# Kernel optimization log

Measured on AMD Instinct MI355X. Metric: run time of the kernel, lower is better.

The kernel has to match this reference:

```python
import jax, jax.numpy as jnp
import numpy as np

DEV_VDW, VDW_N, MAXV, MINV, DM_MIN = 0.2, 6.0, 0.0356, 0.0178, 0.5


def setup_inputs() -> dict:
    key = jax.random.key(0)
    ks = iter(jax.random.split(key, 64))
    B, N1, N2, D, L = 8, 128, 256, 128, 3
    f = jnp.float32
    nrm = lambda shape, s=0.05: jax.random.normal(next(ks), shape, f) * s
    ligand_h = jax.random.normal(next(ks), (B, N1, 54), f)
    target_h = jax.random.normal(next(ks), (B, N2, 54), f)
    def adj(n):
        a = (jax.random.uniform(next(ks), (B, n, n)) < 0.08).astype(f)
        a = jnp.maximum(a, jnp.swapaxes(a, 1, 2))
        return jnp.maximum(a, jnp.eye(n, dtype=f))
    ligand_adj = adj(N1)
    target_adj = adj(N2)
    interaction_indice = jax.random.uniform(next(ks), (B, 3, N1, N2), f)
    ligand_pos = jax.random.normal(next(ks), (B, N1, 3), f) * 2.0
    target_pos = jax.random.normal(next(ks), (B, N2, 3), f) * 4.0
    rotor = jax.random.uniform(next(ks), (B,), f) * 10.0
    ligand_vdw_radii = 1.2 + 0.8 * jax.random.uniform(next(ks), (B, N1), f)
    target_vdw_radii = 1.2 + 0.8 * jax.random.uniform(next(ks), (B, N2), f)
    return dict(
        ligand_h=ligand_h, ligand_adj=ligand_adj, target_h=target_h, target_adj=target_adj,
        interaction_indice=interaction_indice, ligand_pos=ligand_pos, target_pos=target_pos,
        rotor=rotor, ligand_vdw_radii=ligand_vdw_radii, target_vdw_radii=target_vdw_radii,
        ligand_valid=jnp.ones((B, N1), f), target_valid=jnp.ones((B, N2), f),
        ligand_non_metal=jnp.ones((B, N1), f), target_non_metal=jnp.ones((B, N2), f),
        emb_w=nrm((54, D)),
        gat_w=nrm((L, D, D)), gat_b=jnp.zeros((L, D), f), gat_att=nrm((L, D, D)),
        gat_gate_w=nrm((L, 2 * D, 1)), gat_gate_b=jnp.zeros((L, 1), f),
        int_wt_w=nrm((L, D, D)), int_wt_b=jnp.zeros((L, D), f),
        int_mt_w=nrm((L, D, D)), int_mt_b=jnp.zeros((L, D), f),
        gru_w_ih=nrm((L, 3 * D, D)), gru_w_hh=nrm((L, 3 * D, D)),
        gru_b_ih=jnp.zeros((L, 3 * D), f), gru_b_hh=jnp.zeros((L, 3 * D), f),
        A_w1=nrm((2 * D, D)), A_b1=jnp.zeros((D,), f), A_w2=nrm((D, 1)), A_b2=jnp.zeros((1,), f),
        B_w1=nrm((2 * D, D)), B_b1=jnp.zeros((D,), f), B_w2=nrm((D, 1)), B_b2=jnp.zeros((1,), f),
        hbond_coeff=jnp.array([1.0], f), hydrophobic_coeff=jnp.array([0.5], f),
        rotor_coeff=jnp.array([0.5], f),
    )


def reference(ligand_h, ligand_adj, target_h, target_adj, interaction_indice, ligand_pos,
              target_pos, rotor, ligand_vdw_radii, target_vdw_radii, ligand_valid,
              target_valid, ligand_non_metal, target_non_metal, emb_w, gat_w, gat_b,
              gat_att, gat_gate_w, gat_gate_b, int_wt_w, int_wt_b, int_mt_w, int_mt_b,
              gru_w_ih, gru_w_hh, gru_b_ih, gru_b_hh, A_w1, A_b1, A_w2, A_b2, B_w1, B_b1,
              B_w2, B_b2, hbond_coeff, hydrophobic_coeff, rotor_coeff):
    B, D, L = ligand_h.shape[0], emb_w.shape[1], gat_w.shape[0]

    def dist(lpos):
        diff = lpos[:, :, None, :] - target_pos[:, None, :, :]
        dm = jnp.sqrt((diff * diff).sum(-1) + 1e-10)
        return jnp.where(dm < DM_MIN, 1e10, dm)

    dm = dist(ligand_pos)

    def gat(x, adj, i):
        nt = x @ gat_w[i] + gat_b[i]                                   # [B,N,D]
        ea = jnp.einsum('bjl,bkl->bjk', nt @ gat_att[i], nt)
        ea = ea + jnp.swapaxes(ea, 1, 2)
        aw = jax.nn.softmax(jnp.where(adj > 1e-6, ea, -9e15), axis=-1) * adj
        out = jax.nn.relu(jnp.einsum('bij,bjd->bid', aw, nt))
        gate = jax.nn.sigmoid(jnp.concatenate([x, out], -1) @ gat_gate_w[i] + gat_gate_b[i])
        return gate * x + (1.0 - gate) * out

    lh = ligand_h @ emb_w
    th = target_h @ emb_w
    for i in range(L):
        lh = gat(lh, ligand_adj, i)
        th = gat(th, target_adj, i)

    adj12 = jax.lax.stop_gradient(dm)
    adj12 = jnp.where(adj12 > 5.0, 0.0, adj12)
    adj12 = jnp.where(adj12 > 1e-3, 1.0, 0.0)
    adj21 = jnp.swapaxes(adj12, 1, 2)

    def inter(a1, a2, ev, i):
        t1 = a1 @ int_wt_w[i] + int_wt_b[i]
        m2 = a2 @ int_mt_w[i] + int_mt_b[i]                            # [B,N2,D]
        t2 = (m2[:, None, :, :] * ev[..., None]).max(axis=2)           # [B,N1,D]
        msg = jax.nn.relu(t1 + t2)
        gi = msg @ gru_w_ih[i].T + gru_b_ih[i]
        gh = a1 @ gru_w_hh[i].T + gru_b_hh[i]
        i_r, i_z, i_n = jnp.split(gi, 3, -1)
        h_r, h_z, h_n = jnp.split(gh, 3, -1)
        r = jax.nn.sigmoid(i_r + h_r)
        z = jax.nn.sigmoid(i_z + h_z)
        n = jnp.tanh(i_n + r * h_n)
        return (1.0 - z) * n + z * a1

    for i in range(L):
        lh, th = inter(lh, th, adj12, i), inter(th, lh, adj21, i)

    N1, N2 = lh.shape[1], th.shape[1]
    h_cat = jnp.concatenate([
        jnp.broadcast_to(lh[:, :, None, :], (B, N1, N2, D)),
        jnp.broadcast_to(th[:, None, :, :], (B, N1, N2, D))], -1)      # [B,N1,N2,2D]

    A_raw = jax.nn.sigmoid(jax.nn.relu(h_cat @ A_w1 + A_b1) @ A_w2 + A_b2)[..., 0]
    B_raw = jnp.tanh(jax.nn.relu(h_cat @ B_w1 + B_b1) @ B_w2 + B_b2)[..., 0] * DEV_VDW
    dm0 = ligand_vdw_radii[:, :, None] + target_vdw_radii[:, None, :] + B_raw
    valid_pair = ligand_non_metal[:, :, None] * target_non_metal[:, None, :]
    A_vdw = A_raw * (MAXV - MINV) + MINV

    def energies_of(dm):
        dm0c = jnp.where(dm0 < 1e-4, 1.0, dm0)
        r6 = (dm0c / dm) ** VDW_N
        evdw = A_vdw * (jnp.minimum(r6 * r6 - 2.0 * r6, 100.0) * valid_pair)
        vdw_val = evdw.sum((1, 2))[:, None]
        dmd = dm - dm0
        def hb(Aind):
            r = jnp.clip(dmd * Aind / -0.7, 0.0, 1.0) * -(hbond_coeff[0] * hbond_coeff[0])
            return r.sum((1, 2))[:, None]
        hbond = hb(interaction_indice[:, 0])
        metal = hb(interaction_indice[:, 1])
        hp = jnp.clip((-dmd + 1.5) * interaction_indice[:, 2], 0.0, 1.0)
        hp = hp * -(hydrophobic_coeff[0] * hydrophobic_coeff[0])
        e = jnp.concatenate([vdw_val, hbond, metal, hp.sum((1, 2))[:, None]], -1)
        return e / (1.0 + rotor_coeff[0] * rotor_coeff[0] * rotor[:, None])

    energies = energies_of(dm)
    esum = lambda p: energies_of(dist(p)).sum()
    g = jax.grad(esum)(ligand_pos)
    der1 = (g.sum(1) ** 2).mean()
    der2 = -jax.grad(lambda p: jax.grad(esum)(p).sum())(ligand_pos).sum((1, 2)).mean()
    return energies, der1, der2
```

## Files before the change

kernel.cpp:

```cpp
#include <hip/hip_runtime.h>
#include <math.h>

#define BB 8
#define N1C 128
#define N2C 256
#define DC 128
#define NHC 54
#define ROWS_L 1024
#define ROWS_T 2048
#define ROWS_ALL 3072

__device__ __forceinline__ float wredSum(float v) {
#pragma unroll
  for (int o = 32; o > 0; o >>= 1) v += __shfl_down(v, o);
  return v;
}
__device__ float blockSum(float v) {
  __shared__ float red[9];
  v = wredSum(v);
  int lane = threadIdx.x & 63, wid = threadIdx.x >> 6;
  __syncthreads();
  if (lane == 0) red[wid] = v;
  __syncthreads();
  if (threadIdx.x == 0) {
    float s = 0.f;
    int nw = (blockDim.x + 63) >> 6;
    for (int i = 0; i < nw; ++i) s += red[i];
    red[8] = s;
  }
  __syncthreads();
  return red[8];
}

__global__ __launch_bounds__(128) void k_emb(const float* __restrict__ LH,
                                             const float* __restrict__ TH,
                                             const float* __restrict__ W,
                                             float* __restrict__ H0) {
  int r0 = blockIdx.x * 4;
  __shared__ float xs[4][NHC];
  for (int t = threadIdx.x; t < 4 * NHC; t += 128) {
    int rr = r0 + t / NHC, c = t % NHC;
    xs[t / NHC][c] = (rr < ROWS_L) ? LH[(long)rr * NHC + c]
                                   : TH[(long)(rr - ROWS_L) * NHC + c];
  }
  __syncthreads();
  int d = threadIdx.x;
  float a0 = 0.f, a1 = 0.f, a2 = 0.f, a3 = 0.f;
#pragma unroll 6
  for (int k = 0; k < NHC; ++k) {
    float wv = W[(long)k * DC + d];
    a0 += xs[0][k] * wv;
    a1 += xs[1][k] * wv;
    a2 += xs[2][k] * wv;
    a3 += xs[3][k] * wv;
  }
  H0[(long)(r0 + 0) * DC + d] = a0;
  H0[(long)(r0 + 1) * DC + d] = a1;
  H0[(long)(r0 + 2) * DC + d] = a2;
  H0[(long)(r0 + 3) * DC + d] = a3;
}

__global__ __launch_bounds__(128) void k_wfuse(const float* __restrict__ GWp,
                                               const float* __restrict__ GBp,
                                               const float* __restrict__ ATT,
                                               float* __restrict__ WA,
                                               float* __restrict__ bA) {
  int l = blockIdx.y;
  const float* Wl = GWp + (long)l * DC * DC;
  const float* Al = ATT + (long)l * DC * DC;
  int d = threadIdx.x;
  if (blockIdx.x == 32) {
    float acc = 0.f;
#pragma unroll 8
    for (int m = 0; m < DC; ++m) acc += GBp[l * DC + m] * Al[(long)m * DC + d];
    bA[l * DC + d] = acc;
    return;
  }
  int r0 = blockIdx.x * 4;
  __shared__ float xs[4][DC];
  for (int t = threadIdx.x; t < 4 * DC; t += 128)
    xs[t >> 7][t & 127] = Wl[(long)r0 * DC + t];
  __syncthreads();
  float a0 = 0.f, a1 = 0.f, a2 = 0.f, a3 = 0.f;
#pragma unroll 8
  for (int m = 0; m < DC; ++m) {
    float av = Al[(long)m * DC + d];
    a0 += xs[0][m] * av;
    a1 += xs[1][m] * av;
    a2 += xs[2][m] * av;
    a3 += xs[3][m] * av;
  }
  float* out = WA + (long)l * DC * DC + (long)r0 * DC + d;
  out[0] = a0;
  out[DC] = a1;
  out[2 * DC] = a2;
  out[3 * DC] = a3;
}

__global__ __launch_bounds__(256) void k_lin2h(
    const float* __restrict__ X, const float* __restrict__ W1,
    const float* __restrict__ b1, const float* __restrict__ W2,
    const float* __restrict__ b2, float* __restrict__ Y1, float* __restrict__ Y2,
    int rpb, int trans) {
  int r0 = blockIdx.x * 4;
  __shared__ float xs[4][DC];
  int tid = threadIdx.x;
  for (int t = tid; t < 4 * DC; t += 256)
    xs[t >> 7][t & 127] = X[(long)r0 * DC + t];
  __syncthreads();
  int h = tid >> 7, d = tid & 127;
  const float* W = h ? W2 : W1;
  const float* bp = h ? b2 : b1;
  float* Y = h ? Y2 : Y1;
  float a0 = 0.f, a1 = 0.f, a2 = 0.f, a3 = 0.f;
#pragma unroll 16
  for (int k = 0; k < DC; ++k) {
    float wv = W[(long)k * DC + d];
    a0 += xs[0][k] * wv;
    a1 += xs[1][k] * wv;
    a2 += xs[2][k] * wv;
    a3 += xs[3][k] * wv;
  }
  float bv = bp ? bp[d] : 0.f;
  float v[4] = {a0 + bv, a1 + bv, a2 + bv, a3 + bv};
  if (!trans) {
#pragma unroll
    for (int r = 0; r < 4; ++r) Y[(long)(r0 + r) * DC + d] = v[r];
  } else {
    int b = r0 / rpb, rin = r0 - b * rpb;
#pragma unroll
    for (int r = 0; r < 4; ++r)
      Y[((long)b * DC + d) * rpb + rin + r] = v[r];
  }
}

template <int N>
__global__ __launch_bounds__(256) void k_ea(const float* __restrict__ NTp,
                                            const float* __restrict__ E1p,
                                            const float* __restrict__ ADJ,
                                            float* __restrict__ EAp,
                                            int baseRow) {
  const int D = DC;
  int b = blockIdx.z;
  int j0 = blockIdx.y * 16, k0 = blockIdx.x * 16;
  int tj = threadIdx.y, tk = threadIdx.x;
  __shared__ float e1j[16][17], ntj[16][17], e1k[16][17], ntk[16][17];
  const float* E1b = E1p + (long)(baseRow + b * N) * D;
  const float* NTb = NTp + (long)(baseRow + b * N) * D;
  float acc = 0.f;
  for (int kk = 0; kk < D; kk += 16) {
    e1j[tj][tk] = E1b[(long)(j0 + tj) * D + kk + tk];
    ntj[tj][tk] = NTb[(long)(j0 + tj) * D + kk + tk];
    e1k[tj][tk] = E1b[(long)(k0 + tj) * D + kk + tk];
    ntk[tj][tk] = NTb[(long)(k0 + tj) * D + kk + tk];
    __syncthreads();
#pragma unroll
    for (int t = 0; t < 16; ++t)
      acc += e1j[tj][t] * ntk[tk][t] + ntj[tj][t] * e1k[tk][t];
    __syncthreads();
  }
  long idx = (long)b * N * N + (long)(j0 + tj) * N + k0 + tk;
  float ad = ADJ[idx];
  EAp[idx] = (ad > 1e-6f) ? acc : -9e15f;
}

__global__ __launch_bounds__(512) void k_smagg(
    const float* __restrict__ EAL, const float* __restrict__ EAT,
    const float* __restrict__ NTp, const float* __restrict__ Xp,
    const float* __restrict__ GW, const float* __restrict__ GB,
    float* __restrict__ Y) {
  int z = blockIdx.z;
  int N = z ? N2C : N1C;
  if (blockIdx.x * 8 >= N) return;
  int ls = z ? 8 : 7;
  int baseRow = z ? ROWS_L : 0;
  const float* EA = z ? EAT : EAL;
  int b = blockIdx.y, i0 = blockIdx.x * 8;
  __shared__ float ps[8][N2C + 4];
  __shared__ float col[32][DC + 4];
  __shared__ float red[8][2];
  int tid = threadIdx.x;
  const float* EAb = EA + (long)b * N * N + (long)i0 * N;
  for (int t = tid; t < 8 * N; t += 512)
    ps[t >> ls][t & (N - 1)] = EAb[t];
  __syncthreads();
  {
    int r = tid >> 6, l = tid & 63;
    float m = -INFINITY;
    for (int k = l; k < N; k += 64) m = fmaxf(m, ps[r][k]);
#pragma unroll
    for (int o = 32; o > 0; o >>= 1) m = fmaxf(m, __shfl_xor(m, o));
    float s = 0.f;
    for (int k = l; k < N; k += 64) {
      float p = expf(ps[r][k] - m);
      ps[r][k] = p;
      s += p;
    }
#pragma unroll
    for (int o = 32; o > 0; o >>= 1) s += __shfl_xor(s, o);
    float inv = 1.f / s;
    for (int k = l; k < N; k += 64) ps[r][k] *= inv;
  }
  int d = tid & 127, ro = tid >> 7;
  float acc[2] = {0.f, 0.f};
  const float* NTb = NTp + (long)(baseRow + b * N) * DC;
  for (int k0 = 0; k0 < N; k0 += 32) {
    __syncthreads();
    for (int t = tid; t < 32 * DC; t += 512)
      col[t >> 7][t & 127] = NTb[(long)(k0 + (t >> 7)) * DC + (t & 127)];
    __syncthreads();
#pragma unroll 8
    for (int kk = 0; kk < 32; ++kk) {
      float cv = col[kk][d];
      acc[0] = fmaf(ps[ro][k0 + kk], cv, acc[0]);
      acc[1] = fmaf(ps[ro + 4][k0 + kk], cv, acc[1]);
    }
  }
  float gwd = GW[d], gwo = GW[DC + d];
  float xv[2], ov[2], part[2];
#pragma unroll
  for (int q = 0; q < 2; ++q) {
    int r = ro + 4 * q;
    float o = fmaxf(acc[q], 0.f);
    ov[q] = o;
    float x = Xp[(long)(baseRow + b * N + i0 + r) * DC + d];
    xv[q] = x;
    part[q] = x * gwd + o * gwo;
  }
  int wid = tid >> 6;
#pragma unroll
  for (int q = 0; q < 2; ++q) {
    float v = wredSum(part[q]);
    if ((tid & 63) == 0) red[wid][q] = v;
  }
  __syncthreads();
  float gb = GB[0];
#pragma unroll
  for (int q = 0; q < 2; ++q) {
    int r = ro + 4 * q;
    float s = red[2 * ro][q] + red[2 * ro + 1][q];
    float g = 1.f / (1.f + expf(-(s + gb)));
    Y[(long)(baseRow + b * N + i0 + r) * DC + d] = g * xv[q] + (1.f - g) * ov[q];
  }
}

__global__ void k_adj12(const float* __restrict__ LP, const float* __restrict__ TP,
                        float* __restrict__ AD) {
  long idx = (long)blockIdx.x * blockDim.x + threadIdx.x;
  if (idx >= (long)BB * N1C * N2C) return;
  int j = idx & (N2C - 1);
  long t = idx >> 8;
  int i = (int)(t & (N1C - 1));
  int b = (int)(t >> 7);
  float dx = LP[((long)b * N1C + i) * 3 + 0] - TP[((long)b * N2C + j) * 3 + 0];
  float dy = LP[((long)b * N1C + i) * 3 + 1] - TP[((long)b * N2C + j) * 3 + 1];
  float dz = LP[((long)b * N1C + i) * 3 + 2] - TP[((long)b * N2C + j) * 3 + 2];
  float d = sqrtf(dx * dx + dy * dy + dz * dz + 1e-10f);
  if (d < 0.5f) d = 1e10f;
  AD[idx] = (d <= 5.0f && d > 1e-3f) ? 1.f : 0.f;
}

__global__ __launch_bounds__(256) void k_msg2z(const float* __restrict__ T1,
                                               const float* __restrict__ M2,
                                               const float* __restrict__ EV,
                                               float* __restrict__ MSG) {
  int z = blockIdx.z, b = blockIdx.y;
  int Ni = z ? N2C : N1C, Nj = z ? N1C : N2C;
  int t1off = z ? ROWS_L : 0, m2off = z ? 0 : ROWS_L;
  long ev_is = z ? 1L : (long)N2C, ev_js = z ? (long)N2C : 1L;
  int i0 = blockIdx.x * 8;
  if (i0 >= Ni) return;
  __shared__ float m2s[32][DC];
  __shared__ float evs[8][32];
  int d = threadIdx.x & 127, io = threadIdx.x >> 7;
  float acc[4];
#pragma unroll
  for (int q = 0; q < 4; ++q) acc[q] = -INFINITY;
  const float* M2b = M2 + (long)(m2off + b * Nj) * DC;
  const float* EVb = EV + (long)b * (N1C * N2C);
  for (int j0 = 0; j0 < Nj; j0 += 32) {
    __syncthreads();
    for (int t = threadIdx.x; t < 32 * DC; t += 256)
      m2s[t >> 7][t & 127] = M2b[(long)(j0 + (t >> 7)) * DC + (t & 127)];
    for (int t = threadIdx.x; t < 8 * 32; t += 256)
      evs[t >> 5][t & 31] =
          EVb[(long)(i0 + (t >> 5)) * ev_is + (long)(j0 + (t & 31)) * ev_js];
    __syncthreads();
#pragma unroll 8
    for (int jj = 0; jj < 32; ++jj) {
      float m2v = m2s[jj][d];
#pragma unroll
      for (int q = 0; q < 4; ++q)
        acc[q] = fmaxf(acc[q], m2v * evs[io + 2 * q][jj]);
    }
  }
#pragma unroll
  for (int q = 0; q < 4; ++q) {
    int i = i0 + io + 2 * q;
    long row = t1off + (long)b * Ni + i;
    MSG[row * DC + d] = fmaxf(T1[row * DC + d] + acc[q], 0.f);
  }
}

__global__ __launch_bounds__(384) void k_gruf(
    const float* __restrict__ MSGp, const float* __restrict__ Hp,
    const float* __restrict__ WihT, const float* __restrict__ WhhT,
    const float* __restrict__ bih, const float* __restrict__ bhh,
    float* __restrict__ Y) {
  const int D = DC;
  int r0 = blockIdx.x * 4;
  __shared__ float xs_t[DC][4], hs_t[DC][4];
  __shared__ float gis[4][384], ghs[4][384];
  int tid = threadIdx.x;
  for (int t = tid; t < 4 * DC; t += 384) {
    int r = t >> 7, c = t & 127;
    xs_t[c][r] = MSGp[(long)(r0 + r) * D + c];
    hs_t[c][r] = Hp[(long)(r0 + r) * D + c];
  }
  __syncthreads();
  int dd = tid;
  float ai[4] = {0.f, 0.f, 0.f, 0.f}, ah[4] = {0.f, 0.f, 0.f, 0.f};
#pragma unroll 8
  for (int k = 0; k < DC; ++k) {
    float4 xv = *reinterpret_cast<const float4*>(&xs_t[k][0]);
    float4 hv = *reinterpret_cast<const float4*>(&hs_t[k][0]);
    float wi = WihT[(long)k * 384 + dd];
    float wh = WhhT[(long)k * 384 + dd];
    ai[0] = fmaf(xv.x, wi, ai[0]);
    ai[1] = fmaf(xv.y, wi, ai[1]);
    ai[2] = fmaf(xv.z, wi, ai[2]);
    ai[3] = fmaf(xv.w, wi, ai[3]);
    ah[0] = fmaf(hv.x, wh, ah[0]);
    ah[1] = fmaf(hv.y, wh, ah[1]);
    ah[2] = fmaf(hv.z, wh, ah[2]);
    ah[3] = fmaf(hv.w, wh, ah[3]);
  }
  float bi = bih[dd], bh = bhh[dd];
#pragma unroll
  for (int r = 0; r < 4; ++r) {
    gis[r][dd] = ai[r] + bi;
    ghs[r][dd] = ah[r] + bh;
  }
  __syncthreads();
  for (int t = tid; t < 4 * DC; t += 384) {
    int r = t >> 7, d = t & 127;
    float ir = gis[r][d], iz = gis[r][d + 128], inn = gis[r][d + 256];
    float hr = ghs[r][d], hz = ghs[r][d + 128], hn = ghs[r][d + 256];
    float rg = 1.f / (1.f + expf(-(ir + hr)));
    float zg = 1.f / (1.f + expf(-(iz + hz)));
    float ng = tanhf(inn + rg * hn);
    Y[(long)(r0 + r) * D + d] = (1.f - zg) * ng + zg * hs_t[d][r];
  }
}

__global__ void k_tall(const float* __restrict__ IH, const float* __restrict__ HH,
                       float* __restrict__ GIHT, float* __restrict__ GHHT) {
  long idx = (long)blockIdx.x * 256 + threadIdx.x;
  if (idx >= 6L * 49152) return;
  int a = (int)(idx / 49152);
  int rem = (int)(idx % 49152);
  int l = a >> 1, whh = a & 1;
  int c = rem / 384, rr = rem % 384;
  const float* src = (whh ? HH : IH) + (long)l * 49152;
  float* dst = (whh ? GHHT : GIHT) + (long)l * 49152;
  dst[(long)c * 384 + rr] = src[(long)rr * 128 + c];
}

__global__ __launch_bounds__(256) void k_pair(
    const float* __restrict__ UA, const float* __restrict__ VAT,
    const float* __restrict__ UB, const float* __restrict__ VBT,
    const float* __restrict__ AW2, const float* __restrict__ AB2,
    const float* __restrict__ BW2, const float* __restrict__ BB2,
    const float* __restrict__ LP, const float* __restrict__ TP,
    const float* __restrict__ LVDW, const float* __restrict__ TVDW,
    const float* __restrict__ LNM, const float* __restrict__ TNM,
    const float* __restrict__ II, const float* __restrict__ HBC,
    const float* __restrict__ HPC, float* __restrict__ PART) {
  const int D = DC, N1 = N1C, N2 = N2C;
  int i = blockIdx.x, b = blockIdx.y, j = threadIdx.x;
  __shared__ float ua[128], ub[128], wa2[128], wb2[128];
  if (j < 128) {
    long rb = ((long)b * N1 + i) * D + j;
    ua[j] = UA[rb];
    ub[j] = UB[rb];
    wa2[j] = AW2[j];
    wb2[j] = BW2[j];
  }
  __syncthreads();
  const float* vat = VAT + (long)b * D * N2;
  const float* vbt = VBT + (long)b * D * N2;
  float dotA = 0.f, dotB = 0.f;
#pragma unroll 8
  for (int d = 0; d < D; ++d) {
    dotA += fmaxf(ua[d] + vat[(long)d * N2 + j], 0.f) * wa2[d];
    dotB += fmaxf(ub[d] + vbt[(long)d * N2 + j], 0.f) * wb2[d];
  }
  float A_raw = 1.f / (1.f + expf(-(dotA + AB2[0])));
  float A_vdw = A_raw * (0.0356f - 0.0178f) + 0.0178f;
  float B_raw = tanhf(dotB + BB2[0]) * 0.2f;

  float lx = LP[((long)b * N1 + i) * 3 + 0];
  float ly = LP[((long)b * N1 + i) * 3 + 1];
  float lz = LP[((long)b * N1 + i) * 3 + 2];
  float tx = TP[((long)b * N2 + j) * 3 + 0];
  float ty = TP[((long)b * N2 + j) * 3 + 1];
  float tz = TP[((long)b * N2 + j) * 3 + 2];
  float dx = lx - tx, dy = ly - ty, dz = lz - tz;
  float s2 = dx * dx + dy * dy + dz * dz + 1e-10f;
  float draw = sqrtf(s2);
  bool clamped = draw < 0.5f;
  float dmv = clamped ? 1e10f : draw;

  float dm0 = LVDW[b * N1 + i] + TVDW[b * N2 + j] + B_raw;
  float dm0c = (dm0 < 1e-4f) ? 1.f : dm0;
  float valid = LNM[b * N1 + i] * TNM[b * N2 + j];

  float rr = dm0c / dmv;
  float r2 = rr * rr, r6 = r2 * r2 * r2;
  float fv = r6 * r6 - 2.f * r6;
  float evdw = A_vdw * (fminf(fv, 100.f) * valid);

  float dmd = dmv - dm0;
  long ii0 = ((long)b * 3) * N1 * N2 + (long)i * N2 + j;
  float I0 = II[ii0];
  float I1 = II[ii0 + (long)N1 * N2];
  float I2 = II[ii0 + 2L * N1 * N2];
  float hb2 = HBC[0] * HBC[0], hp2 = HPC[0] * HPC[0];
  float u0 = dmd * I0 / (-0.7f);
  float u1 = dmd * I1 / (-0.7f);
  float vv = (1.5f - dmd) * I2;
  float ehb = fminf(fmaxf(u0, 0.f), 1.f) * (-hb2);
  float emt = fminf(fmaxf(u1, 0.f), 1.f) * (-hb2);
  float ehp = fminf(fmaxf(vv, 0.f), 1.f) * (-hp2);

  float gx = 0.f, gy = 0.f, gz = 0.f, d2t = 0.f;
  if (!clamped) {
    float Ep = 0.f, Epp = 0.f;
    if (fv < 100.f) {
      float c = A_vdw * valid;
      Ep += c * (-12.f) * r6 * (r6 - 1.f) / draw;
      Epp += c * r6 * (156.f * r6 - 84.f) / s2;
    }
    if (u0 > 0.f && u0 < 1.f) Ep += hb2 * I0 * (1.f / 0.7f);
    if (u1 > 0.f && u1 < 1.f) Ep += hb2 * I1 * (1.f / 0.7f);
    if (vv > 0.f && vv < 1.f) Ep += hp2 * I2;
    float invd = 1.f / draw;
    gx = Ep * dx * invd;
    gy = Ep * dy * invd;
    gz = Ep * dz * invd;
    float T = dx + dy + dz;
    float tt = T * T / s2;
    d2t = Epp * tt + Ep * (3.f - tt) * invd;
  }

  float o0 = blockSum(evdw);
  float o1 = blockSum(ehb);
  float o2 = blockSum(emt);
  float o3 = blockSum(ehp);
  float o4 = blockSum(gx);
  float o5 = blockSum(gy);
  float o6 = blockSum(gz);
  float o7 = blockSum(d2t);
  if (j == 0) {
    float* p = PART + ((long)b * N1 + i) * 8;
    p[0] = o0; p[1] = o1; p[2] = o2; p[3] = o3;
    p[4] = o4; p[5] = o5; p[6] = o6; p[7] = o7;
  }
}

__global__ void k_final(const float* __restrict__ PART, const float* __restrict__ ROT,
                        const float* __restrict__ RC, float* __restrict__ OUT) {
  const int N1 = N1C;
  __shared__ float s[8][8];
  int t = threadIdx.x;
  if (t < 64) {
    int b = t >> 3, k1 = t & 7;
    float acc = 0.f;
    for (int i = 0; i < N1; ++i) acc += PART[((long)b * N1 + i) * 8 + k1];
    s[b][k1] = acc;
  }
  __syncthreads();
  if (t == 0) {
    float rcc = RC[0] * RC[0];
    float der1 = 0.f, der2 = 0.f;
    for (int b = 0; b < 8; ++b) {
      float w = 1.f / (1.f + rcc * ROT[b]);
      OUT[b * 4 + 0] = s[b][0] * w;
      OUT[b * 4 + 1] = s[b][1] * w;
      OUT[b * 4 + 2] = s[b][2] * w;
      OUT[b * 4 + 3] = s[b][3] * w;
      for (int c = 0; c < 3; ++c) {
        float S = s[b][4 + c] * w;
        der1 += S * S;
      }
      der2 += s[b][7] * w;
    }
    OUT[32] = der1 / 24.f;
    OUT[33] = -der2 / 8.f;
  }
}

extern "C" void kernel_launch(void* const* d_in, const int* in_sizes, int n_in,
                              void* d_out, int out_size, void* d_ws, size_t ws_size,
                              hipStream_t stream) {
  (void)in_sizes; (void)n_in; (void)out_size; (void)ws_size;
  const int D = DC;

  const float* ligand_h   = (const float*)d_in[0];
  const float* ligand_adj = (const float*)d_in[1];
  const float* target_h   = (const float*)d_in[2];
  const float* target_adj = (const float*)d_in[3];
  const float* inter_ind  = (const float*)d_in[4];
  const float* ligand_pos = (const float*)d_in[5];
  const float* target_pos = (const float*)d_in[6];
  const float* rotor      = (const float*)d_in[7];
  const float* lvdw       = (const float*)d_in[8];
  const float* tvdw       = (const float*)d_in[9];
  const float* lnm        = (const float*)d_in[12];
  const float* tnm        = (const float*)d_in[13];
  const float* emb_w      = (const float*)d_in[14];
  const float* gat_w      = (const float*)d_in[15];
  const float* gat_b      = (const float*)d_in[16];
  const float* gat_att    = (const float*)d_in[17];
  const float* gat_gate_w = (const float*)d_in[18];
  const float* gat_gate_b = (const float*)d_in[19];
  const float* int_wt_w   = (const float*)d_in[20];
  const float* int_wt_b   = (const float*)d_in[21];
  const float* int_mt_w   = (const float*)d_in[22];
  const float* int_mt_b   = (const float*)d_in[23];
  const float* gru_w_ih   = (const float*)d_in[24];
  const float* gru_w_hh   = (const float*)d_in[25];
  const float* gru_b_ih   = (const float*)d_in[26];
  const float* gru_b_hh   = (const float*)d_in[27];
  const float* A_w1       = (const float*)d_in[28];
  const float* A_b1       = (const float*)d_in[29];
  const float* A_w2       = (const float*)d_in[30];
  const float* A_b2       = (const float*)d_in[31];
  const float* B_w1       = (const float*)d_in[32];
  const float* B_b1       = (const float*)d_in[33];
  const float* B_w2       = (const float*)d_in[34];
  const float* B_b2       = (const float*)d_in[35];
  const float* hb_c       = (const float*)d_in[36];
  const float* hp_c       = (const float*)d_in[37];
  const float* rc_c       = (const float*)d_in[38];

  float* w = (float*)d_ws;
  auto take = [&](size_t n) { float* p = w; w += n; return p; };
  float* H0    = take((size_t)ROWS_ALL * DC);
  float* H1    = take((size_t)ROWS_ALL * DC);
  float* NT    = take((size_t)ROWS_ALL * DC);
  float* E1    = take((size_t)ROWS_ALL * DC);
  float* EAL   = take((size_t)BB * N1C * N1C);
  float* EAT   = take((size_t)BB * N2C * N2C);
  float* ADJ12 = take((size_t)BB * N1C * N2C);
  float* WA    = take((size_t)3 * DC * DC);
  float* bA    = take((size_t)3 * DC);
  float* GIHT  = take((size_t)3 * DC * 384);
  float* GHHT  = take((size_t)3 * DC * 384);
  float* PART  = take((size_t)BB * N1C * 8);
  float* T1  = NT;
  float* M2  = E1;
  float* MSG = EAT;
  float* UA  = EAL;
  float* UB  = EAT;
  float* VAT = NT;
  float* VBT = E1;

  k_adj12<<<(BB * N1C * N2C + 255) / 256, 256, 0, stream>>>(ligand_pos,
                                                            target_pos, ADJ12);
  k_emb<<<ROWS_ALL / 4, 128, 0, stream>>>(ligand_h, target_h, emb_w, H0);
  k_wfuse<<<dim3(33, 3), 128, 0, stream>>>(gat_w, gat_b, gat_att, WA, bA);

  float *cur = H0, *alt = H1;

  for (int l = 0; l < 3; ++l) {
    k_lin2h<<<ROWS_ALL / 4, 256, 0, stream>>>(
        cur, gat_w + (size_t)l * D * D, gat_b + l * D, WA + (size_t)l * D * D,
        bA + l * D, NT, E1, 1, 0);
    k_ea<N1C><<<dim3(N1C / 16, N1C / 16, BB), dim3(16, 16), 0, stream>>>(
        NT, E1, ligand_adj, EAL, 0);
    k_ea<N2C><<<dim3(N2C / 16, N2C / 16, BB), dim3(16, 16), 0, stream>>>(
        NT, E1, target_adj, EAT, ROWS_L);
    k_smagg<<<dim3(N2C / 8, BB, 2), 512, 0, stream>>>(
        EAL, EAT, NT, cur, gat_gate_w + l * 2 * D, gat_gate_b + l, alt);
    float* t = cur; cur = alt; alt = t;
  }

  k_tall<<<(6 * 49152 + 255) / 256, 256, 0, stream>>>(gru_w_ih, gru_w_hh, GIHT,
                                                      GHHT);

  for (int l = 0; l < 3; ++l) {
    k_lin2h<<<ROWS_ALL / 4, 256, 0, stream>>>(
        cur, int_wt_w + (size_t)l * D * D, int_wt_b + l * D,
        int_mt_w + (size_t)l * D * D, int_mt_b + l * D, T1, M2, 1, 0);
    k_msg2z<<<dim3(N2C / 8, BB, 2), 256, 0, stream>>>(T1, M2, ADJ12, MSG);
    k_gruf<<<ROWS_ALL / 4, 384, 0, stream>>>(MSG, cur, GIHT + (size_t)l * D * 384,
                                             GHHT + (size_t)l * D * 384,
                                             gru_b_ih + l * 384,
                                             gru_b_hh + l * 384, alt);
    float* t = cur; cur = alt; alt = t;
  }

  k_lin2h<<<ROWS_L / 4, 256, 0, stream>>>(cur, A_w1, A_b1, B_w1, B_b1, UA, UB,
                                          1, 0);
  k_lin2h<<<ROWS_T / 4, 256, 0, stream>>>(cur + (size_t)ROWS_L * DC,
                                          A_w1 + D * D, nullptr, B_w1 + D * D,
                                          nullptr, VAT, VBT, N2C, 1);

  k_pair<<<dim3(N1C, BB), 256, 0, stream>>>(UA, VAT, UB, VBT, A_w2, A_b2, B_w2,
                                            B_b2, ligand_pos, target_pos, lvdw,
                                            tvdw, lnm, tnm, inter_ind, hb_c,
                                            hp_c, PART);

  k_final<<<1, 256, 0, stream>>>(PART, rotor, rc_c, (float*)d_out);
}
```

Before: 374.0 us.

## Merge prep kernels, register-tile attention GEMM, vectorize msg and lin2h inner loops

```diff
diff --git a/kernel.cpp b/kernel.cpp
--- a/kernel.cpp
+++ b/kernel.cpp
@@ -32,69 +32,96 @@
   return red[8];
 }
 
-__global__ __launch_bounds__(128) void k_emb(const float* __restrict__ LH,
-                                             const float* __restrict__ TH,
-                                             const float* __restrict__ W,
-                                             float* __restrict__ H0) {
-  int r0 = blockIdx.x * 4;
-  __shared__ float xs[4][NHC];
-  for (int t = threadIdx.x; t < 4 * NHC; t += 128) {
-    int rr = r0 + t / NHC, c = t % NHC;
-    xs[t / NHC][c] = (rr < ROWS_L) ? LH[(long)rr * NHC + c]
-                                   : TH[(long)(rr - ROWS_L) * NHC + c];
-  }
-  __syncthreads();
-  int d = threadIdx.x;
-  float a0 = 0.f, a1 = 0.f, a2 = 0.f, a3 = 0.f;
+__global__ __launch_bounds__(256) void k_prep(
+    const float* __restrict__ LP, const float* __restrict__ TP,
+    float* __restrict__ AD, const float* __restrict__ LH,
+    const float* __restrict__ TH, const float* __restrict__ EW,
+    float* __restrict__ H0, const float* __restrict__ GWp,
+    const float* __restrict__ GBp, const float* __restrict__ ATT,
+    float* __restrict__ WA, float* __restrict__ bA,
+    const float* __restrict__ IH, const float* __restrict__ HH,
+    float* __restrict__ GIHT, float* __restrict__ GHHT) {
+  int bid = blockIdx.x, tid = threadIdx.x;
+  if (bid < 1024) {
+    long idx = (long)bid * 256 + tid;
+    int j = idx & (N2C - 1);
+    long t = idx >> 8;
+    int i = (int)(t & (N1C - 1));
+    int b = (int)(t >> 7);
+    float dx = LP[((long)b * N1C + i) * 3 + 0] - TP[((long)b * N2C + j) * 3 + 0];
+    float dy = LP[((long)b * N1C + i) * 3 + 1] - TP[((long)b * N2C + j) * 3 + 1];
+    float dz = LP[((long)b * N1C + i) * 3 + 2] - TP[((long)b * N2C + j) * 3 + 2];
+    float d = sqrtf(dx * dx + dy * dy + dz * dz + 1e-10f);
+    if (d < 0.5f) d = 1e10f;
+    AD[idx] = (d <= 5.0f && d > 1e-3f) ? 1.f : 0.f;
+  } else if (bid < 1024 + 384) {
+    int r0 = (bid - 1024) * 8;
+    __shared__ float xs[8][NHC];
+    for (int t = tid; t < 8 * NHC; t += 256) {
+      int rr = r0 + t / NHC, c = t % NHC;
+      xs[t / NHC][c] = (rr < ROWS_L) ? LH[(long)rr * NHC + c]
+                                     : TH[(long)(rr - ROWS_L) * NHC + c];
+    }
+    __syncthreads();
+    int d = tid & 127, rb = (tid >> 7) * 4;
+    float a[4] = {0.f, 0.f, 0.f, 0.f};
 #pragma unroll 6
-  for (int k = 0; k < NHC; ++k) {
-    float wv = W[(long)k * DC + d];
-    a0 += xs[0][k] * wv;
-    a1 += xs[1][k] * wv;
-    a2 += xs[2][k] * wv;
-    a3 += xs[3][k] * wv;
-  }
-  H0[(long)(r0 + 0) * DC + d] = a0;
-  H0[(long)(r0 + 1) * DC + d] = a1;
-  H0[(long)(r0 + 2) * DC + d] = a2;
-  H0[(long)(r0 + 3) * DC + d] = a3;
-}
-
-__global__ __launch_bounds__(128) void k_wfuse(const float* __restrict__ GWp,
-                                               const float* __restrict__ GBp,
-                                               const float* __restrict__ ATT,
-                                               float* __restrict__ WA,
-                                               float* __restrict__ bA) {
-  int l = blockIdx.y;
-  const float* Wl = GWp + (long)l * DC * DC;
-  const float* Al = ATT + (long)l * DC * DC;
-  int d = threadIdx.x;
-  if (blockIdx.x == 32) {
-    float acc = 0.f;
+    for (int k = 0; k < NHC; ++k) {
+      float wv = EW[(long)k * DC + d];
+#pragma unroll
+      for (int r = 0; r < 4; ++r) a[r] += xs[rb + r][k] * wv;
+    }
+#pragma unroll
+    for (int r = 0; r < 4; ++r) H0[(long)(r0 + rb + r) * DC + d] = a[r];
+  } else if (bid < 1024 + 384 + 99) {
+    int q = bid - 1408;
+    int l = q / 33, bx = q % 33;
+    const float* Wl = GWp + (long)l * DC * DC;
+    const float* Al = ATT + (long)l * DC * DC;
+    if (bx == 32) {
+      if (tid < 128) {
+        float acc = 0.f;
 #pragma unroll 8
-    for (int m = 0; m < DC; ++m) acc += GBp[l * DC + m] * Al[(long)m * DC + d];
-    bA[l * DC + d] = acc;
-    return;
-  }
-  int r0 = blockIdx.x * 4;
-  __shared__ float xs[4][DC];
-  for (int t = threadIdx.x; t < 4 * DC; t += 128)
-    xs[t >> 7][t & 127] = Wl[(long)r0 * DC + t];
-  __syncthreads();
-  float a0 = 0.f, a1 = 0.f, a2 = 0.f, a3 = 0.f;
+        for (int m = 0; m < DC; ++m)
+          acc += GBp[l * DC + m] * Al[(long)m * DC + tid];
+        bA[l * DC + tid] = acc;
+      }
+    } else {
+      __shared__ float xs2[4][DC];
+      int r0 = bx * 4;
+      for (int t = tid; t < 4 * DC; t += 256)
+        xs2[t >> 7][t & 127] = Wl[(long)r0 * DC + t];
+      __syncthreads();
+      if (tid < 128) {
+        int d = tid;
+        float a0 = 0.f, a1 = 0.f, a2 = 0.f, a3 = 0.f;
 #pragma unroll 8
-  for (int m = 0; m < DC; ++m) {
-    float av = Al[(long)m * DC + d];
-    a0 += xs[0][m] * av;
-    a1 += xs[1][m] * av;
-    a2 += xs[2][m] * av;
-    a3 += xs[3][m] * av;
-  }
-  float* out = WA + (long)l * DC * DC + (long)r0 * DC + d;
-  out[0] = a0;
-  out[DC] = a1;
-  out[2 * DC] = a2;
-  out[3 * DC] = a3;
+        for (int m = 0; m < DC; ++m) {
+          float av = Al[(long)m * DC + d];
+          a0 += xs2[0][m] * av;
+          a1 += xs2[1][m] * av;
+          a2 += xs2[2][m] * av;
+          a3 += xs2[3][m] * av;
+        }
+        float* out = WA + (long)l * DC * DC + (long)r0 * DC + d;
+        out[0] = a0;
+        out[DC] = a1;
+        out[2 * DC] = a2;
+        out[3 * DC] = a3;
+      }
+    }
+  } else {
+    long idx = (long)(bid - 1507) * 256 + tid;
+    if (idx < 6L * 49152) {
+      int a = (int)(idx / 49152);
+      int rem = (int)(idx % 49152);
+      int l = a >> 1, whh = a & 1;
+      int c = rem / 384, rr = rem % 384;
+      const float* src = (whh ? HH : IH) + (long)l * 49152;
+      float* dst = (whh ? GHHT : GIHT) + (long)l * 49152;
+      dst[(long)c * 384 + rr] = src[(long)rr * 128 + c];
+    }
+  }
 }
 
 __global__ __launch_bounds__(256) void k_lin2h(
@@ -103,23 +130,26 @@
     const float* __restrict__ b2, float* __restrict__ Y1, float* __restrict__ Y2,
     int rpb, int trans) {
   int r0 = blockIdx.x * 4;
-  __shared__ float xs[4][DC];
+  __shared__ float xs_t[DC][4];
   int tid = threadIdx.x;
-  for (int t = tid; t < 4 * DC; t += 256)
-    xs[t >> 7][t & 127] = X[(long)r0 * DC + t];
+  for (int t = tid; t < 4 * DC; t += 256) {
+    int r = t >> 7, c = t & 127;
+    xs_t[c][r] = X[(long)(r0 + r) * DC + c];
+  }
   __syncthreads();
   int h = tid >> 7, d = tid & 127;
   const float* W = h ? W2 : W1;
   const float* bp = h ? b2 : b1;
   float* Y = h ? Y2 : Y1;
   float a0 = 0.f, a1 = 0.f, a2 = 0.f, a3 = 0.f;
-#pragma unroll 16
+#pragma unroll 8
   for (int k = 0; k < DC; ++k) {
+    float4 xv = *(const float4*)&xs_t[k][0];
     float wv = W[(long)k * DC + d];
-    a0 += xs[0][k] * wv;
-    a1 += xs[1][k] * wv;
-    a2 += xs[2][k] * wv;
-    a3 += xs[3][k] * wv;
+    a0 = fmaf(xv.x, wv, a0);
+    a1 = fmaf(xv.y, wv, a1);
+    a2 = fmaf(xv.z, wv, a2);
+    a3 = fmaf(xv.w, wv, a3);
   }
   float bv = bp ? bp[d] : 0.f;
   float v[4] = {a0 + bv, a1 + bv, a2 + bv, a3 + bv};
@@ -134,34 +164,84 @@
   }
 }
 
-template <int N>
-__global__ __launch_bounds__(256) void k_ea(const float* __restrict__ NTp,
-                                            const float* __restrict__ E1p,
-                                            const float* __restrict__ ADJ,
-                                            float* __restrict__ EAp,
-                                            int baseRow) {
-  const int D = DC;
-  int b = blockIdx.z;
-  int j0 = blockIdx.y * 16, k0 = blockIdx.x * 16;
-  int tj = threadIdx.y, tk = threadIdx.x;
-  __shared__ float e1j[16][17], ntj[16][17], e1k[16][17], ntk[16][17];
-  const float* E1b = E1p + (long)(baseRow + b * N) * D;
-  const float* NTb = NTp + (long)(baseRow + b * N) * D;
-  float acc = 0.f;
-  for (int kk = 0; kk < D; kk += 16) {
-    e1j[tj][tk] = E1b[(long)(j0 + tj) * D + kk + tk];
-    ntj[tj][tk] = NTb[(long)(j0 + tj) * D + kk + tk];
-    e1k[tj][tk] = E1b[(long)(k0 + tj) * D + kk + tk];
-    ntk[tj][tk] = NTb[(long)(k0 + tj) * D + kk + tk];
+__global__ __launch_bounds__(256) void k_ea2(const float* __restrict__ NTp,
+                                             const float* __restrict__ E1p,
+                                             const float* __restrict__ ADJL,
+                                             const float* __restrict__ ADJT,
+                                             float* __restrict__ EAL,
+                                             float* __restrict__ EAT) {
+  int id = blockIdx.x;
+  int N, base, j0, k0, b;
+  const float* ADJ;
+  float* EA;
+  if (id < 64) {
+    b = id >> 3;
+    int rem = id & 7;
+    N = N1C;
+    base = b * N1C;
+    j0 = (rem >> 1) * 32;
+    k0 = (rem & 1) * 64;
+    ADJ = ADJL + (long)b * N1C * N1C;
+    EA = EAL + (long)b * N1C * N1C;
+  } else {
+    int q = id - 64;
+    b = q >> 5;
+    int rem = q & 31;
+    N = N2C;
+    base = ROWS_L + b * N2C;
+    j0 = (rem >> 2) * 32;
+    k0 = (rem & 3) * 64;
+    ADJ = ADJT + (long)b * N2C * N2C;
+    EA = EAT + (long)b * N2C * N2C;
+  }
+  __shared__ float aj_e1[32][34], aj_nt[32][34];
+  __shared__ float bk_e1[32][68], bk_nt[32][68];
+  int tid = threadIdx.x, tx = tid & 15, ty = tid >> 4;
+  float acc[2][4];
+#pragma unroll
+  for (int r = 0; r < 2; ++r)
+#pragma unroll
+    for (int c = 0; c < 4; ++c) acc[r][c] = 0.f;
+  for (int kc = 0; kc < DC; kc += 32) {
     __syncthreads();
-#pragma unroll
-    for (int t = 0; t < 16; ++t)
-      acc += e1j[tj][t] * ntk[tk][t] + ntj[tj][t] * e1k[tk][t];
+    for (int t = tid; t < 1024; t += 256) {
+      int kk = t & 31, rr = t >> 5;
+      aj_e1[kk][rr] = E1p[(long)(base + j0 + rr) * DC + kc + kk];
+      aj_nt[kk][rr] = NTp[(long)(base + j0 + rr) * DC + kc + kk];
+    }
+    for (int t = tid; t < 2048; t += 256) {
+      int kk = t & 31, cc = t >> 5;
+      bk_e1[kk][cc] = E1p[(long)(base + k0 + cc) * DC + kc + kk];
+      bk_nt[kk][cc] = NTp[(long)(base + k0 + cc) * DC + kc + kk];
+    }
     __syncthreads();
-  }
-  long idx = (long)b * N * N + (long)(j0 + tj) * N + k0 + tk;
-  float ad = ADJ[idx];
-  EAp[idx] = (ad > 1e-6f) ? acc : -9e15f;
+#pragma unroll
+    for (int kk = 0; kk < 32; ++kk) {
+      float2 ae = *(const float2*)&aj_e1[kk][ty * 2];
+      float2 an = *(const float2*)&aj_nt[kk][ty * 2];
+      float4 bn = *(const float4*)&bk_nt[kk][tx * 4];
+      float4 be = *(const float4*)&bk_e1[kk][tx * 4];
+      acc[0][0] = fmaf(ae.x, bn.x, fmaf(an.x, be.x, acc[0][0]));
+      acc[0][1] = fmaf(ae.x, bn.y, fmaf(an.x, be.y, acc[0][1]));
+      acc[0][2] = fmaf(ae.x, bn.z, fmaf(an.x, be.z, acc[0][2]));
+      acc[0][3] = fmaf(ae.x, bn.w, fmaf(an.x, be.w, acc[0][3]));
+      acc[1][0] = fmaf(ae.y, bn.x, fmaf(an.y, be.x, acc[1][0]));
+      acc[1][1] = fmaf(ae.y, bn.y, fmaf(an.y, be.y, acc[1][1]));
+      acc[1][2] = fmaf(ae.y, bn.z, fmaf(an.y, be.z, acc[1][2]));
+      acc[1][3] = fmaf(ae.y, bn.w, fmaf(an.y, be.w, acc[1][3]));
+    }
+  }
+#pragma unroll
+  for (int r = 0; r < 2; ++r) {
+    long rowi = (long)(j0 + ty * 2 + r) * N + k0 + tx * 4;
+    float4 ad = *(const float4*)&ADJ[rowi];
+    float4 o;
+    o.x = (ad.x > 1e-6f) ? acc[r][0] : -9e15f;
+    o.y = (ad.y > 1e-6f) ? acc[r][1] : -9e15f;
+    o.z = (ad.z > 1e-6f) ? acc[r][2] : -9e15f;
+    o.w = (ad.w > 1e-6f) ? acc[r][3] : -9e15f;
+    *(float4*)&EA[rowi] = o;
+  }
 }
 
 __global__ __launch_bounds__(512) void k_smagg(
@@ -244,62 +324,49 @@
   }
 }
 
-__global__ void k_adj12(const float* __restrict__ LP, const float* __restrict__ TP,
-                        float* __restrict__ AD) {
-  long idx = (long)blockIdx.x * blockDim.x + threadIdx.x;
-  if (idx >= (long)BB * N1C * N2C) return;
-  int j = idx & (N2C - 1);
-  long t = idx >> 8;
-  int i = (int)(t & (N1C - 1));
-  int b = (int)(t >> 7);
-  float dx = LP[((long)b * N1C + i) * 3 + 0] - TP[((long)b * N2C + j) * 3 + 0];
-  float dy = LP[((long)b * N1C + i) * 3 + 1] - TP[((long)b * N2C + j) * 3 + 1];
-  float dz = LP[((long)b * N1C + i) * 3 + 2] - TP[((long)b * N2C + j) * 3 + 2];
-  float d = sqrtf(dx * dx + dy * dy + dz * dz + 1e-10f);
-  if (d < 0.5f) d = 1e10f;
-  AD[idx] = (d <= 5.0f && d > 1e-3f) ? 1.f : 0.f;
-}
-
-__global__ __launch_bounds__(256) void k_msg2z(const float* __restrict__ T1,
+__global__ __launch_bounds__(256) void k_msg2v(const float* __restrict__ T1,
                                                const float* __restrict__ M2,
                                                const float* __restrict__ EV,
                                                float* __restrict__ MSG) {
   int z = blockIdx.z, b = blockIdx.y;
   int Ni = z ? N2C : N1C, Nj = z ? N1C : N2C;
+  if (blockIdx.x * 8 >= Ni) return;
   int t1off = z ? ROWS_L : 0, m2off = z ? 0 : ROWS_L;
   long ev_is = z ? 1L : (long)N2C, ev_js = z ? (long)N2C : 1L;
   int i0 = blockIdx.x * 8;
-  if (i0 >= Ni) return;
-  __shared__ float m2s[32][DC];
-  __shared__ float evs[8][32];
-  int d = threadIdx.x & 127, io = threadIdx.x >> 7;
-  float acc[4];
-#pragma unroll
-  for (int q = 0; q < 4; ++q) acc[q] = -INFINITY;
+  __shared__ float m2s[32][DC + 4];
+  __shared__ float evs[8][36];
+  int dgrp = threadIdx.x & 31, row = threadIdx.x >> 5;
+  int d0 = dgrp * 4;
+  float a0 = -INFINITY, a1 = -INFINITY, a2 = -INFINITY, a3 = -INFINITY;
   const float* M2b = M2 + (long)(m2off + b * Nj) * DC;
   const float* EVb = EV + (long)b * (N1C * N2C);
   for (int j0 = 0; j0 < Nj; j0 += 32) {
     __syncthreads();
     for (int t = threadIdx.x; t < 32 * DC; t += 256)
       m2s[t >> 7][t & 127] = M2b[(long)(j0 + (t >> 7)) * DC + (t & 127)];
-    for (int t = threadIdx.x; t < 8 * 32; t += 256)
+    for (int t = threadIdx.x; t < 256; t += 256)
       evs[t >> 5][t & 31] =
           EVb[(long)(i0 + (t >> 5)) * ev_is + (long)(j0 + (t & 31)) * ev_js];
     __syncthreads();
 #pragma unroll 8
     for (int jj = 0; jj < 32; ++jj) {
-      float m2v = m2s[jj][d];
-#pragma unroll
-      for (int q = 0; q < 4; ++q)
-        acc[q] = fmaxf(acc[q], m2v * evs[io + 2 * q][jj]);
-    }
-  }
-#pragma unroll
-  for (int q = 0; q < 4; ++q) {
-    int i = i0 + io + 2 * q;
-    long row = t1off + (long)b * Ni + i;
-    MSG[row * DC + d] = fmaxf(T1[row * DC + d] + acc[q], 0.f);
-  }
+      float4 m4 = *(const float4*)&m2s[jj][d0];
+      float e = evs[row][jj];
+      a0 = fmaxf(a0, m4.x * e);
+      a1 = fmaxf(a1, m4.y * e);
+      a2 = fmaxf(a2, m4.z * e);
+      a3 = fmaxf(a3, m4.w * e);
+    }
+  }
+  long grow = t1off + (long)b * Ni + i0 + row;
+  float4 t4 = *(const float4*)&T1[grow * DC + d0];
+  float4 o;
+  o.x = fmaxf(t4.x + a0, 0.f);
+  o.y = fmaxf(t4.y + a1, 0.f);
+  o.z = fmaxf(t4.z + a2, 0.f);
+  o.w = fmaxf(t4.w + a3, 0.f);
+  *(float4*)&MSG[grow * DC + d0] = o;
 }
 
 __global__ __launch_bounds__(384) void k_gruf(
@@ -351,19 +418,6 @@
     float ng = tanhf(inn + rg * hn);
     Y[(long)(r0 + r) * D + d] = (1.f - zg) * ng + zg * hs_t[d][r];
   }
-}
-
-__global__ void k_tall(const float* __restrict__ IH, const float* __restrict__ HH,
-                       float* __restrict__ GIHT, float* __restrict__ GHHT) {
-  long idx = (long)blockIdx.x * 256 + threadIdx.x;
-  if (idx >= 6L * 49152) return;
-  int a = (int)(idx / 49152);
-  int rem = (int)(idx % 49152);
-  int l = a >> 1, whh = a & 1;
-  int c = rem / 384, rr = rem % 384;
-  const float* src = (whh ? HH : IH) + (long)l * 49152;
-  float* dst = (whh ? GHHT : GIHT) + (long)l * 49152;
-  dst[(long)c * 384 + rr] = src[(long)rr * 128 + c];
 }
 
 __global__ __launch_bounds__(256) void k_pair(
@@ -566,10 +620,9 @@
   float* VAT = NT;
   float* VBT = E1;
 
-  k_adj12<<<(BB * N1C * N2C + 255) / 256, 256, 0, stream>>>(ligand_pos,
-                                                            target_pos, ADJ12);
-  k_emb<<<ROWS_ALL / 4, 128, 0, stream>>>(ligand_h, target_h, emb_w, H0);
-  k_wfuse<<<dim3(33, 3), 128, 0, stream>>>(gat_w, gat_b, gat_att, WA, bA);
+  k_prep<<<2659, 256, 0, stream>>>(ligand_pos, target_pos, ADJ12, ligand_h,
+                                   target_h, emb_w, H0, gat_w, gat_b, gat_att,
+                                   WA, bA, gru_w_ih, gru_w_hh, GIHT, GHHT);
 
   float *cur = H0, *alt = H1;
 
@@ -577,23 +630,17 @@
     k_lin2h<<<ROWS_ALL / 4, 256, 0, stream>>>(
         cur, gat_w + (size_t)l * D * D, gat_b + l * D, WA + (size_t)l * D * D,
         bA + l * D, NT, E1, 1, 0);
-    k_ea<N1C><<<dim3(N1C / 16, N1C / 16, BB), dim3(16, 16), 0, stream>>>(
-        NT, E1, ligand_adj, EAL, 0);
-    k_ea<N2C><<<dim3(N2C / 16, N2C / 16, BB), dim3(16, 16), 0, stream>>>(
-        NT, E1, target_adj, EAT, ROWS_L);
+    k_ea2<<<320, 256, 0, stream>>>(NT, E1, ligand_adj, target_adj, EAL, EAT);
     k_smagg<<<dim3(N2C / 8, BB, 2), 512, 0, stream>>>(
         EAL, EAT, NT, cur, gat_gate_w + l * 2 * D, gat_gate_b + l, alt);
     float* t = cur; cur = alt; alt = t;
   }
-
-  k_tall<<<(6 * 49152 + 255) / 256, 256, 0, stream>>>(gru_w_ih, gru_w_hh, GIHT,
-                                                      GHHT);
 
   for (int l = 0; l < 3; ++l) {
     k_lin2h<<<ROWS_ALL / 4, 256, 0, stream>>>(
         cur, int_wt_w + (size_t)l * D * D, int_wt_b + l * D,
         int_mt_w + (size_t)l * D * D, int_mt_b + l * D, T1, M2, 1, 0);
-    k_msg2z<<<dim3(N2C / 8, BB, 2), 256, 0, stream>>>(T1, M2, ADJ12, MSG);
+    k_msg2v<<<dim3(32, 8, 2), 256, 0, stream>>>(T1, M2, ADJ12, MSG);
     k_gruf<<<ROWS_ALL / 4, 384, 0, stream>>>(MSG, cur, GIHT + (size_t)l * D * 384,
                                              GHHT + (size_t)l * D * 384,
                                              gru_b_ih + l * 384,
```

Measured after the change: 351.2 us. 6.1% less time.
